# Kernel tuning notes

Hardware: AMD Instinct MI355X
Metric: run time of the kernel (lower is better)

The kernel has to match this reference:

```python
import jax, jax.numpy as jnp
import numpy as np
import math

DIM = 1024
NUM_HEADS = 16
HEAD_DIM = DIM // NUM_HEADS
B, S = 2, 2048

def setup_inputs() -> dict:
    key = jax.random.key(0)
    ks = jax.random.split(key, 9)
    sc = 0.02
    return {
        "x": jax.random.normal(ks[0], (B, S, DIM), jnp.float32),
        "Wq": jax.random.normal(ks[1], (DIM, DIM), jnp.float32) * sc,
        "bq": jax.random.normal(ks[2], (DIM,), jnp.float32) * sc,
        "Wk": jax.random.normal(ks[3], (DIM, DIM), jnp.float32) * sc,
        "bk": jax.random.normal(ks[4], (DIM,), jnp.float32) * sc,
        "Wv": jax.random.normal(ks[5], (DIM, DIM), jnp.float32) * sc,
        "bv": jax.random.normal(ks[6], (DIM,), jnp.float32) * sc,
        "Wo": jax.random.normal(ks[7], (DIM, DIM), jnp.float32) * sc,
        "bo": jax.random.normal(ks[8], (DIM,), jnp.float32) * sc,
    }

def reference(x, Wq, bq, Wk, bk, Wv, bv, Wo, bo):
    b, s, d = x.shape
    h, hd = NUM_HEADS, HEAD_DIM
    # qkv projections: [B,S,D] -> [B,H,S,hd]
    def split_heads(t):
        return t.reshape(b, s, h, hd).transpose(0, 2, 1, 3)
    q = split_heads(x @ Wq + bq)
    k = split_heads(x @ Wk + bk)
    v = split_heads(x @ Wv + bv)
    # scores [B,H,S,S], scale, causal mask via where(-10000), softmax
    scores = jnp.einsum('bhqd,bhkd->bhqk', q, k) / math.sqrt(hd)
    causal = jnp.tril(jnp.ones((s, s), dtype=bool))  # [S,S]
    scores = jnp.where(causal[None, None], scores, jnp.asarray(-10000.0, scores.dtype))
    probs = jax.nn.softmax(scores, axis=-1)
    ctx = jnp.einsum('bhqk,bhkd->bhqd', probs, v)
    ctx = ctx.transpose(0, 2, 1, 3).reshape(b, s, d)
    return ctx @ Wo + bo
```

## Files before the change

### kernel.cpp

```cpp
#include <hip/hip_runtime.h>
#include <hip/hip_bf16.h>

#define DIM 1024
#define NUM_HEADS 16
#define HEAD_DIM 64
#define BATCH 2
#define SEQ 2048
#define M_ROWS (BATCH * SEQ)

typedef short bh8 __attribute__((ext_vector_type(8)));
typedef float f32x4 __attribute__((ext_vector_type(4)));

__device__ __forceinline__ ushort f2bf(float f) {
    union { float f; unsigned u; } v; v.f = f;
    unsigned u = v.u;
    unsigned r = (u + 0x7FFFu + ((u >> 16) & 1u)) >> 16;
    return (ushort)r;
}

__device__ __forceinline__ ushort2 pk_bf16(float a, float b) {
#if __has_builtin(__builtin_amdgcn_cvt_pk_bf16_f32)
    auto r = __builtin_amdgcn_cvt_pk_bf16_f32(a, b);
    ushort2 o; __builtin_memcpy(&o, &r, 4); return o;
#else
    ushort2 o; o.x = f2bf(a); o.y = f2bf(b); return o;
#endif
}

__device__ __forceinline__ void async_cp16(const ushort* g, ushort* l) {
    __builtin_amdgcn_global_load_lds(
        (const __attribute__((address_space(1))) void*)(uintptr_t)g,
        (__attribute__((address_space(3))) void*)(uint32_t)(uintptr_t)l,
        16, 0, 0);
}

__global__ __launch_bounds__(256) void cast_x(const float* __restrict__ in,
                                              ushort* __restrict__ out, int n4) {
    int i = blockIdx.x * 256 + threadIdx.x;
    if (i < n4) {
        float4 v = ((const float4*)in)[i];
        ushort4 o;
        o.x = f2bf(v.x); o.y = f2bf(v.y); o.z = f2bf(v.z); o.w = f2bf(v.w);
        ((ushort4*)out)[i] = o;
    }
}

__global__ __launch_bounds__(256) void transpose_cast(const float* __restrict__ W,
                                                      ushort* __restrict__ Wt) {
    __shared__ float tile[32][33];
    const int t = threadIdx.x;
    const int tx = t & 31, ty = t >> 5;
    const int k0 = blockIdx.y * 32, n0 = blockIdx.x * 32;
    #pragma unroll
    for (int i = 0; i < 4; ++i)
        tile[ty + 8 * i][tx] = W[(size_t)(k0 + ty + 8 * i) * DIM + n0 + tx];
    __syncthreads();
    #pragma unroll
    for (int i = 0; i < 4; ++i)
        Wt[(size_t)(n0 + ty + 8 * i) * DIM + k0 + tx] = f2bf(tile[tx][ty + 8 * i]);
}

#define GTM 128
#define GTN 64
#define GBK 64

__device__ __forceinline__ void gemm_core(
    const ushort* __restrict__ A, const ushort* __restrict__ Bt,
    ushort* smem, int m0, int n0, int t, f32x4 acc[4][2])
{
    ushort* As = smem;
    ushort* Bs = smem + 8192;
    const int lane = t & 63, wave = t >> 6;
    const int col = lane & 15, quad = lane >> 4;
    const int wm = (wave & 1) * 64, wn = (wave >> 1) * 32;

    for (int k0 = 0; k0 < DIM; k0 += GBK) {
        __syncthreads();
        #pragma unroll
        for (int j = 0; j < 4; ++j) {
            int C = wave * 256 + j * 64 + lane;
            int row = C >> 3;
            int lch = (C & 7) ^ (row & 7);
            async_cp16(&A[(size_t)(m0 + row) * DIM + k0 + lch * 8],
                       &As[(wave * 256 + j * 64) * 8]);
        }
        #pragma unroll
        for (int j = 0; j < 2; ++j) {
            int C = wave * 128 + j * 64 + lane;
            int row = C >> 3;
            int lch = (C & 7) ^ (row & 7);
            async_cp16(&Bt[(size_t)(n0 + row) * DIM + k0 + lch * 8],
                       &Bs[(wave * 128 + j * 64) * 8]);
        }
        __syncthreads();
        #pragma unroll
        for (int kk = 0; kk < 2; ++kk) {
            bh8 af[4], bfr[2];
            #pragma unroll
            for (int mi = 0; mi < 4; ++mi) {
                int row = wm + mi * 16 + col;
                int ph = ((kk * 4 + quad) ^ (row & 7)) * 8;
                af[mi] = *(const bh8*)&As[row * 64 + ph];
            }
            #pragma unroll
            for (int ni = 0; ni < 2; ++ni) {
                int row = wn + ni * 16 + col;
                int ph = ((kk * 4 + quad) ^ (row & 7)) * 8;
                bfr[ni] = *(const bh8*)&Bs[row * 64 + ph];
            }
            #pragma unroll
            for (int mi = 0; mi < 4; ++mi)
                #pragma unroll
                for (int ni = 0; ni < 2; ++ni)
                    acc[mi][ni] = __builtin_amdgcn_mfma_f32_16x16x32_bf16(
                        af[mi], bfr[ni], acc[mi][ni], 0, 0, 0);
        }
    }
}

__global__ __launch_bounds__(256) void gemm_qkv(
    const ushort* __restrict__ A,
    const ushort* __restrict__ WqT, const ushort* __restrict__ WkT,
    const ushort* __restrict__ WvT,
    const float* __restrict__ bq, const float* __restrict__ bk,
    const float* __restrict__ bv,
    ushort* __restrict__ qo, ushort* __restrict__ ko_, ushort* __restrict__ vo)
{
    __shared__ ushort smem[12288];
    const int z = blockIdx.z;
    const ushort* Bt = (z == 0) ? WqT : (z == 1) ? WkT : WvT;
    const float* bias = (z == 0) ? bq : (z == 1) ? bk : bv;
    ushort* outp = (z == 0) ? qo : (z == 1) ? ko_ : vo;

    const int t = threadIdx.x;
    const int lane = t & 63, wave = t >> 6;
    const int col = lane & 15, quad = lane >> 4;
    const int m0 = blockIdx.y * GTM, n0 = blockIdx.x * GTN;
    const int wm = (wave & 1) * 64, wn = (wave >> 1) * 32;
    f32x4 acc[4][2] = {};

    gemm_core(A, Bt, smem, m0, n0, t, acc);

    const int b = m0 >> 11, s0 = m0 & (SEQ - 1);
    const int h = n0 >> 6;

    if (z < 2) {
        __syncthreads();
        ushort* LT = smem;
        #pragma unroll
        for (int mi = 0; mi < 4; ++mi)
            #pragma unroll
            for (int ni = 0; ni < 2; ++ni) {
                int dl = wn + ni * 16 + col;
                float bvv = bias[n0 + dl];
                #pragma unroll
                for (int r = 0; r < 4; ++r) {
                    int ml = wm + mi * 16 + quad * 4 + r;
                    LT[ml * 72 + dl] = f2bf(acc[mi][ni][r] + bvv);
                }
            }
        __syncthreads();
        ushort* Cp = outp + (((size_t)(b * NUM_HEADS + h) * SEQ + s0) << 6);
        #pragma unroll
        for (int i = 0; i < 4; ++i) {
            int c = i * 256 + t;
            int row = c >> 3, ko = (c & 7) * 8;
            *(uint4*)&Cp[row * 64 + ko] = *(const uint4*)&LT[row * 72 + ko];
        }
    } else {
        __syncthreads();
        ushort* LT = smem;
        #pragma unroll
        for (int mi = 0; mi < 4; ++mi)
            #pragma unroll
            for (int ni = 0; ni < 2; ++ni) {
                int nl = wn + ni * 16 + col;
                float bvv = bias[n0 + nl];
                #pragma unroll
                for (int r = 0; r < 4; ++r) {
                    int ml = wm + mi * 16 + quad * 4 + r;
                    LT[nl * 136 + ml] = f2bf(acc[mi][ni][r] + bvv);
                }
            }
        __syncthreads();
        ushort* Cp = outp + (((size_t)(b * NUM_HEADS + h) * HEAD_DIM) << 11);
        #pragma unroll
        for (int i = 0; i < 4; ++i) {
            int c = i * 256 + t;
            int row = c >> 4, mo = (c & 15) * 8;
            *(uint4*)&Cp[((size_t)row << 11) + s0 + mo] = *(const uint4*)&LT[row * 136 + mo];
        }
    }
}

__global__ __launch_bounds__(256) void gemm_out(
    const ushort* __restrict__ A, const ushort* __restrict__ Bt,
    const float* __restrict__ bias, float* __restrict__ C)
{
    __shared__ ushort smem[12288];
    const int t = threadIdx.x;
    const int lane = t & 63, wave = t >> 6;
    const int col = lane & 15, quad = lane >> 4;
    const int m0 = blockIdx.y * GTM, n0 = blockIdx.x * GTN;
    const int wm = (wave & 1) * 64, wn = (wave >> 1) * 32;
    f32x4 acc[4][2] = {};

    gemm_core(A, Bt, smem, m0, n0, t, acc);

    #pragma unroll
    for (int mi = 0; mi < 4; ++mi)
        #pragma unroll
        for (int ni = 0; ni < 2; ++ni) {
            int n = n0 + wn + ni * 16 + col;
            float bvv = bias[n];
            #pragma unroll
            for (int r = 0; r < 4; ++r) {
                int m = m0 + wm + mi * 16 + quad * 4 + r;
                C[(size_t)m * DIM + n] = acc[mi][ni][r] + bvv;
            }
        }
}

#define PSTR 72

__global__ __launch_bounds__(256) void attn_mfma(
    const ushort* __restrict__ Qg, const ushort* __restrict__ Kg,
    const ushort* __restrict__ Vtg, ushort* __restrict__ ctx)
{
    __shared__ ushort Ks[64 * 64];
    __shared__ ushort Vs[64 * 64];
    __shared__ ushort Ps[4][16 * PSTR];

    const int t = threadIdx.x;
    const int lane = t & 63, wave = t >> 6;
    const int col = lane & 15, quad = lane >> 4;
    const int pair = blockIdx.x & 15;
    const int bh = blockIdx.x >> 4;
    const int b = bh >> 4, h = bh & 15;
    const ushort* Kp = Kg + ((size_t)bh << 17);
    const ushort* Vp = Vtg + ((size_t)bh << 17);
    ushort* Pw = Ps[wave];
    const float SCL = 0.18033688011116016f;

    #pragma unroll 1
    for (int phase = 0; phase < 2; ++phase) {
        const int qt = phase ? (31 - pair) : pair;
        const int q0 = qt * 64;
        const int qw = q0 + wave * 16;

        bh8 qf0, qf1;
        {
            const ushort* Qp = Qg + ((size_t)bh << 17) + ((size_t)(qw + col) << 6) + quad * 8;
            qf0 = *(const bh8*)(Qp);
            qf1 = *(const bh8*)(Qp + 32);
        }
        float m_run = -1e30f, l_run = 0.f;
        f32x4 O[4] = {};

        #pragma unroll 1
        for (int kb = 0; kb <= q0; kb += 64) {
            __syncthreads();
            #pragma unroll
            for (int j = 0; j < 2; ++j) {
                int C = wave * 128 + j * 64 + lane;
                int row = C >> 3;
                int lch = (C & 7) ^ (row & 7);
                async_cp16(&Kp[((size_t)(kb + row) << 6) + lch * 8],
                           &Ks[(wave * 128 + j * 64) * 8]);
                async_cp16(&Vp[((size_t)row << 11) + kb + lch * 8],
                           &Vs[(wave * 128 + j * 64) * 8]);
            }
            __syncthreads();

            f32x4 St[4] = {};
            #pragma unroll
            for (int kk = 0; kk < 2; ++kk) {
                bh8 qf = kk ? qf1 : qf0;
                int ph = ((kk * 4 + quad) ^ (col & 7)) * 8;
                #pragma unroll
                for (int kt = 0; kt < 4; ++kt) {
                    bh8 kf = *(const bh8*)&Ks[(kt * 16 + col) * 64 + ph];
                    St[kt] = __builtin_amdgcn_mfma_f32_16x16x32_bf16(kf, qf, St[kt], 0, 0, 0);
                }
            }

            if (kb == q0) {
                const int q_abs = qw + col;
                #pragma unroll
                for (int kt = 0; kt < 4; ++kt)
                    #pragma unroll
                    for (int r = 0; r < 4; ++r)
                        if (kb + kt * 16 + quad * 4 + r > q_abs) St[kt][r] = -1e30f;
            }

            float mb = -1e30f;
            #pragma unroll
            for (int kt = 0; kt < 4; ++kt) {
                float m01 = fmaxf(St[kt][0], St[kt][1]);
                float m23 = fmaxf(St[kt][2], St[kt][3]);
                mb = fmaxf(mb, fmaxf(m01, m23));
            }
            mb = fmaxf(mb, __shfl_xor(mb, 16));
            mb = fmaxf(mb, __shfl_xor(mb, 32));
            float mn = fmaxf(m_run, mb);
            float alpha = exp2f((m_run - mn) * SCL);
            float negc = -mn * SCL;
            m_run = mn;

            float lb = 0.f;
            #pragma unroll
            for (int kt = 0; kt < 4; ++kt) {
                float p0 = exp2f(fmaf(St[kt][0], SCL, negc));
                float p1 = exp2f(fmaf(St[kt][1], SCL, negc));
                float p2 = exp2f(fmaf(St[kt][2], SCL, negc));
                float p3 = exp2f(fmaf(St[kt][3], SCL, negc));
                lb += (p0 + p1) + (p2 + p3);
                ushort2 a01 = pk_bf16(p0, p1), a23 = pk_bf16(p2, p3);
                ushort4 pk4; pk4.x = a01.x; pk4.y = a01.y; pk4.z = a23.x; pk4.w = a23.y;
                *(ushort4*)&Pw[col * PSTR + kt * 16 + quad * 4] = pk4;
            }
            lb += __shfl_xor(lb, 16);
            lb += __shfl_xor(lb, 32);
            l_run = l_run * alpha + lb;

            #pragma unroll
            for (int dt = 0; dt < 4; ++dt)
                #pragma unroll
                for (int r = 0; r < 4; ++r)
                    O[dt][r] *= alpha;

            #pragma unroll
            for (int kk = 0; kk < 2; ++kk) {
                int koff = kk * 32 + quad * 8;
                bh8 pf = *(const bh8*)&Pw[col * PSTR + koff];
                int ph = ((kk * 4 + quad) ^ (col & 7)) * 8;
                #pragma unroll
                for (int dt = 0; dt < 4; ++dt) {
                    bh8 vf = *(const bh8*)&Vs[(dt * 16 + col) * 64 + ph];
                    O[dt] = __builtin_amdgcn_mfma_f32_16x16x32_bf16(vf, pf, O[dt], 0, 0, 0);
                }
            }
        }

        float inv_l = 1.f / l_run;
        #pragma unroll
        for (int dt = 0; dt < 4; ++dt) {
            ushort2 a01 = pk_bf16(O[dt][0] * inv_l, O[dt][1] * inv_l);
            ushort2 a23 = pk_bf16(O[dt][2] * inv_l, O[dt][3] * inv_l);
            ushort4 pk4; pk4.x = a01.x; pk4.y = a01.y; pk4.z = a23.x; pk4.w = a23.y;
            *(ushort4*)&Pw[col * PSTR + dt * 16 + quad * 4] = pk4;
        }
        #pragma unroll
        for (int i = 0; i < 2; ++i) {
            int c = i * 64 + lane;
            int row = c >> 3, ko = (c & 7) * 8;
            *(uint4*)&ctx[((size_t)(b * SEQ) + qw + row) * DIM + (h << 6) + ko] =
                *(const uint4*)&Pw[row * PSTR + ko];
        }
    }
}

extern "C" void kernel_launch(void* const* d_in, const int* in_sizes, int n_in,
                              void* d_out, int out_size, void* d_ws, size_t ws_size,
                              hipStream_t stream) {
    const float* x  = (const float*)d_in[0];
    const float* Wq = (const float*)d_in[1];
    const float* bq = (const float*)d_in[2];
    const float* Wk = (const float*)d_in[3];
    const float* bk = (const float*)d_in[4];
    const float* Wv = (const float*)d_in[5];
    const float* bv = (const float*)d_in[6];
    const float* Wo = (const float*)d_in[7];
    const float* bo = (const float*)d_in[8];
    float* out = (float*)d_out;

    ushort* x_bf   = (ushort*)d_ws;
    ushort* wq_t   = x_bf + 4194304;
    ushort* wk_t   = wq_t + 1048576;
    ushort* wv_t   = wk_t + 1048576;
    ushort* wo_t   = wv_t + 1048576;
    ushort* q_ws   = wo_t + 1048576;
    ushort* k_ws   = q_ws + 4194304;
    ushort* vt_ws  = k_ws + 4194304;
    ushort* ctx_ws = vt_ws + 4194304;

    cast_x<<<4096, 256, 0, stream>>>(x, x_bf, (M_ROWS * DIM) / 4);
    dim3 tgrid(32, 32);
    transpose_cast<<<tgrid, 256, 0, stream>>>(Wq, wq_t);
    transpose_cast<<<tgrid, 256, 0, stream>>>(Wk, wk_t);
    transpose_cast<<<tgrid, 256, 0, stream>>>(Wv, wv_t);
    transpose_cast<<<tgrid, 256, 0, stream>>>(Wo, wo_t);

    dim3 qkv_grid(DIM / GTN, M_ROWS / GTM, 3);
    gemm_qkv<<<qkv_grid, 256, 0, stream>>>(x_bf, wq_t, wk_t, wv_t,
                                           bq, bk, bv, q_ws, k_ws, vt_ws);

    attn_mfma<<<BATCH * NUM_HEADS * 16, 256, 0, stream>>>(q_ws, k_ws, vt_ws, ctx_ws);

    dim3 ogrid(DIM / GTN, M_ROWS / GTM);
    gemm_out<<<ogrid, 256, 0, stream>>>(ctx_ws, wo_t, bo, out);
}
```

Measured before the change: 206.4 us.

## Enlarge GEMM tiles, widen attention query tiles, double-buffer K/V, drop running max

Both projection GEMMs go from 128x64 to 128x128 tiles, so each wave computes a 4x4 MFMA block and there is more reuse per staged tile. The attention kernel now covers 32 query rows per wave (128 per block) with half as many blocks. It double-buffers K/V tiles in LDS and prefetches the next tile while computing the current one. Online softmax max tracking and rescaling are removed, with raw scores exponentiated directly; this drops per-iteration reductions and rescales but risks overflow for inputs with large scores.

```diff
diff --git a/kernel.cpp b/kernel.cpp
--- a/kernel.cpp
+++ b/kernel.cpp
@@ -61,18 +61,18 @@
 }
 
 #define GTM 128
-#define GTN 64
+#define GTN 128
 #define GBK 64
 
 __device__ __forceinline__ void gemm_core(
     const ushort* __restrict__ A, const ushort* __restrict__ Bt,
-    ushort* smem, int m0, int n0, int t, f32x4 acc[4][2])
+    ushort* smem, int m0, int n0, int t, f32x4 acc[4][4])
 {
     ushort* As = smem;
     ushort* Bs = smem + 8192;
     const int lane = t & 63, wave = t >> 6;
     const int col = lane & 15, quad = lane >> 4;
-    const int wm = (wave & 1) * 64, wn = (wave >> 1) * 32;
+    const int wm = (wave & 1) * 64, wn = (wave >> 1) * 64;
 
     for (int k0 = 0; k0 < DIM; k0 += GBK) {
         __syncthreads();
@@ -85,35 +85,33 @@
                        &As[(wave * 256 + j * 64) * 8]);
         }
         #pragma unroll
-        for (int j = 0; j < 2; ++j) {
-            int C = wave * 128 + j * 64 + lane;
+        for (int j = 0; j < 4; ++j) {
+            int C = wave * 256 + j * 64 + lane;
             int row = C >> 3;
             int lch = (C & 7) ^ (row & 7);
             async_cp16(&Bt[(size_t)(n0 + row) * DIM + k0 + lch * 8],
-                       &Bs[(wave * 128 + j * 64) * 8]);
+                       &Bs[(wave * 256 + j * 64) * 8]);
         }
         __syncthreads();
         #pragma unroll
         for (int kk = 0; kk < 2; ++kk) {
-            bh8 af[4], bfr[2];
+            bh8 af[4], bf[4];
             #pragma unroll
             for (int mi = 0; mi < 4; ++mi) {
                 int row = wm + mi * 16 + col;
-                int ph = ((kk * 4 + quad) ^ (row & 7)) * 8;
-                af[mi] = *(const bh8*)&As[row * 64 + ph];
-            }
-            #pragma unroll
-            for (int ni = 0; ni < 2; ++ni) {
+                af[mi] = *(const bh8*)&As[row * 64 + (((kk * 4 + quad) ^ (row & 7)) * 8)];
+            }
+            #pragma unroll
+            for (int ni = 0; ni < 4; ++ni) {
                 int row = wn + ni * 16 + col;
-                int ph = ((kk * 4 + quad) ^ (row & 7)) * 8;
-                bfr[ni] = *(const bh8*)&Bs[row * 64 + ph];
+                bf[ni] = *(const bh8*)&Bs[row * 64 + (((kk * 4 + quad) ^ (row & 7)) * 8)];
             }
             #pragma unroll
             for (int mi = 0; mi < 4; ++mi)
                 #pragma unroll
-                for (int ni = 0; ni < 2; ++ni)
+                for (int ni = 0; ni < 4; ++ni)
                     acc[mi][ni] = __builtin_amdgcn_mfma_f32_16x16x32_bf16(
-                        af[mi], bfr[ni], acc[mi][ni], 0, 0, 0);
+                        af[mi], bf[ni], acc[mi][ni], 0, 0, 0);
         }
     }
 }
@@ -126,7 +124,7 @@
     const float* __restrict__ bv,
     ushort* __restrict__ qo, ushort* __restrict__ ko_, ushort* __restrict__ vo)
 {
-    __shared__ ushort smem[12288];
+    __shared__ ushort smem[17408];
     const int z = blockIdx.z;
     const ushort* Bt = (z == 0) ? WqT : (z == 1) ? WkT : WvT;
     const float* bias = (z == 0) ? bq : (z == 1) ? bk : bv;
@@ -136,59 +134,57 @@
     const int lane = t & 63, wave = t >> 6;
     const int col = lane & 15, quad = lane >> 4;
     const int m0 = blockIdx.y * GTM, n0 = blockIdx.x * GTN;
-    const int wm = (wave & 1) * 64, wn = (wave >> 1) * 32;
-    f32x4 acc[4][2] = {};
+    const int wm = (wave & 1) * 64, wn = (wave >> 1) * 64;
+    f32x4 acc[4][4] = {};
 
     gemm_core(A, Bt, smem, m0, n0, t, acc);
 
     const int b = m0 >> 11, s0 = m0 & (SEQ - 1);
-    const int h = n0 >> 6;
+    const int h0 = n0 >> 6;
+    __syncthreads();
+    ushort* LT = smem;
 
     if (z < 2) {
-        __syncthreads();
-        ushort* LT = smem;
         #pragma unroll
         for (int mi = 0; mi < 4; ++mi)
             #pragma unroll
-            for (int ni = 0; ni < 2; ++ni) {
+            for (int ni = 0; ni < 4; ++ni) {
                 int dl = wn + ni * 16 + col;
                 float bvv = bias[n0 + dl];
                 #pragma unroll
-                for (int r = 0; r < 4; ++r) {
-                    int ml = wm + mi * 16 + quad * 4 + r;
-                    LT[ml * 72 + dl] = f2bf(acc[mi][ni][r] + bvv);
-                }
+                for (int r = 0; r < 4; ++r)
+                    LT[(wm + mi * 16 + quad * 4 + r) * 136 + dl] = f2bf(acc[mi][ni][r] + bvv);
             }
         __syncthreads();
-        ushort* Cp = outp + (((size_t)(b * NUM_HEADS + h) * SEQ + s0) << 6);
-        #pragma unroll
-        for (int i = 0; i < 4; ++i) {
+        #pragma unroll
+        for (int i = 0; i < 8; ++i) {
             int c = i * 256 + t;
-            int row = c >> 3, ko = (c & 7) * 8;
-            *(uint4*)&Cp[row * 64 + ko] = *(const uint4*)&LT[row * 72 + ko];
+            int row = c >> 4;
+            int dcol = (c & 15) * 8;
+            int h = h0 + (dcol >> 6);
+            *(uint4*)&outp[(((size_t)(b * NUM_HEADS + h) * SEQ) + s0 + row) * 64 + (dcol & 63)] =
+                *(const uint4*)&LT[row * 136 + dcol];
         }
     } else {
-        __syncthreads();
-        ushort* LT = smem;
         #pragma unroll
         for (int mi = 0; mi < 4; ++mi)
             #pragma unroll
-            for (int ni = 0; ni < 2; ++ni) {
+            for (int ni = 0; ni < 4; ++ni) {
                 int nl = wn + ni * 16 + col;
                 float bvv = bias[n0 + nl];
                 #pragma unroll
-                for (int r = 0; r < 4; ++r) {
-                    int ml = wm + mi * 16 + quad * 4 + r;
-                    LT[nl * 136 + ml] = f2bf(acc[mi][ni][r] + bvv);
-                }
+                for (int r = 0; r < 4; ++r)
+                    LT[nl * 136 + (wm + mi * 16 + quad * 4 + r)] = f2bf(acc[mi][ni][r] + bvv);
             }
         __syncthreads();
-        ushort* Cp = outp + (((size_t)(b * NUM_HEADS + h) * HEAD_DIM) << 11);
-        #pragma unroll
-        for (int i = 0; i < 4; ++i) {
+        #pragma unroll
+        for (int i = 0; i < 8; ++i) {
             int c = i * 256 + t;
-            int row = c >> 4, mo = (c & 15) * 8;
-            *(uint4*)&Cp[((size_t)row << 11) + s0 + mo] = *(const uint4*)&LT[row * 136 + mo];
+            int row = c >> 4;
+            int moff = (c & 15) * 8;
+            int h = h0 + (row >> 6);
+            *(uint4*)&outp[(((size_t)(b * NUM_HEADS + h) * HEAD_DIM) + (row & 63)) * SEQ + s0 + moff] =
+                *(const uint4*)&LT[row * 136 + moff];
         }
     }
 }
@@ -197,20 +193,20 @@
     const ushort* __restrict__ A, const ushort* __restrict__ Bt,
     const float* __restrict__ bias, float* __restrict__ C)
 {
-    __shared__ ushort smem[12288];
+    __shared__ ushort smem[16384];
     const int t = threadIdx.x;
     const int lane = t & 63, wave = t >> 6;
     const int col = lane & 15, quad = lane >> 4;
     const int m0 = blockIdx.y * GTM, n0 = blockIdx.x * GTN;
-    const int wm = (wave & 1) * 64, wn = (wave >> 1) * 32;
-    f32x4 acc[4][2] = {};
+    const int wm = (wave & 1) * 64, wn = (wave >> 1) * 64;
+    f32x4 acc[4][4] = {};
 
     gemm_core(A, Bt, smem, m0, n0, t, acc);
 
     #pragma unroll
     for (int mi = 0; mi < 4; ++mi)
         #pragma unroll
-        for (int ni = 0; ni < 2; ++ni) {
+        for (int ni = 0; ni < 4; ++ni) {
             int n = n0 + wn + ni * 16 + col;
             float bvv = bias[n];
             #pragma unroll
@@ -227,15 +223,15 @@
     const ushort* __restrict__ Qg, const ushort* __restrict__ Kg,
     const ushort* __restrict__ Vtg, ushort* __restrict__ ctx)
 {
-    __shared__ ushort Ks[64 * 64];
-    __shared__ ushort Vs[64 * 64];
-    __shared__ ushort Ps[4][16 * PSTR];
+    __shared__ ushort Ks[2][64 * 64];
+    __shared__ ushort Vs[2][64 * 64];
+    __shared__ ushort Ps[4][32 * PSTR];
 
     const int t = threadIdx.x;
     const int lane = t & 63, wave = t >> 6;
     const int col = lane & 15, quad = lane >> 4;
-    const int pair = blockIdx.x & 15;
-    const int bh = blockIdx.x >> 4;
+    const int pair = blockIdx.x & 7;
+    const int bh = blockIdx.x >> 3;
     const int b = bh >> 4, h = bh & 15;
     const ushort* Kp = Kg + ((size_t)bh << 17);
     const ushort* Vp = Vtg + ((size_t)bh << 17);
@@ -244,114 +240,128 @@
 
     #pragma unroll 1
     for (int phase = 0; phase < 2; ++phase) {
-        const int qt = phase ? (31 - pair) : pair;
-        const int q0 = qt * 64;
-        const int qw = q0 + wave * 16;
-
-        bh8 qf0, qf1;
+        const int qt = phase ? (15 - pair) : pair;
+        const int q0 = qt * 128;
+        const int qw = q0 + wave * 32;
+
+        bh8 qf[2][2];
+        #pragma unroll
+        for (int ni = 0; ni < 2; ++ni) {
+            const ushort* Qp = Qg + ((size_t)bh << 17) + ((size_t)(qw + ni * 16 + col) << 6) + quad * 8;
+            qf[ni][0] = *(const bh8*)(Qp);
+            qf[ni][1] = *(const bh8*)(Qp + 32);
+        }
+        float l0 = 0.f, l1 = 0.f;
+        f32x4 O[4][2] = {};
+        const int nIter = 2 * qt + 2;
+
+        __syncthreads();
         {
-            const ushort* Qp = Qg + ((size_t)bh << 17) + ((size_t)(qw + col) << 6) + quad * 8;
-            qf0 = *(const bh8*)(Qp);
-            qf1 = *(const bh8*)(Qp + 32);
-        }
-        float m_run = -1e30f, l_run = 0.f;
-        f32x4 O[4] = {};
-
-        #pragma unroll 1
-        for (int kb = 0; kb <= q0; kb += 64) {
-            __syncthreads();
             #pragma unroll
             for (int j = 0; j < 2; ++j) {
                 int C = wave * 128 + j * 64 + lane;
                 int row = C >> 3;
                 int lch = (C & 7) ^ (row & 7);
-                async_cp16(&Kp[((size_t)(kb + row) << 6) + lch * 8],
-                           &Ks[(wave * 128 + j * 64) * 8]);
-                async_cp16(&Vp[((size_t)row << 11) + kb + lch * 8],
-                           &Vs[(wave * 128 + j * 64) * 8]);
-            }
+                async_cp16(&Kp[((size_t)row << 6) + lch * 8], &Ks[0][(wave * 128 + j * 64) * 8]);
+                async_cp16(&Vp[((size_t)row << 11) + lch * 8], &Vs[0][(wave * 128 + j * 64) * 8]);
+            }
+        }
+
+        #pragma unroll 1
+        for (int it = 0; it < nIter; ++it) {
+            const int kb = it * 64;
             __syncthreads();
-
-            f32x4 St[4] = {};
+            if (it + 1 < nIter) {
+                int kb2 = kb + 64;
+                #pragma unroll
+                for (int j = 0; j < 2; ++j) {
+                    int C = wave * 128 + j * 64 + lane;
+                    int row = C >> 3;
+                    int lch = (C & 7) ^ (row & 7);
+                    ushort* kd = &Ks[(it + 1) & 1][(wave * 128 + j * 64) * 8];
+                    ushort* vd = &Vs[(it + 1) & 1][(wave * 128 + j * 64) * 8];
+                    async_cp16(&Kp[((size_t)(kb2 + row) << 6) + lch * 8], kd);
+                    async_cp16(&Vp[((size_t)row << 11) + kb2 + lch * 8], vd);
+                }
+            }
+            if (kb > qw + 31) continue;
+            const ushort* Kb = Ks[it & 1];
+            const ushort* Vb = Vs[it & 1];
+
+            f32x4 St[4][2] = {};
             #pragma unroll
             for (int kk = 0; kk < 2; ++kk) {
-                bh8 qf = kk ? qf1 : qf0;
                 int ph = ((kk * 4 + quad) ^ (col & 7)) * 8;
                 #pragma unroll
                 for (int kt = 0; kt < 4; ++kt) {
-                    bh8 kf = *(const bh8*)&Ks[(kt * 16 + col) * 64 + ph];
-                    St[kt] = __builtin_amdgcn_mfma_f32_16x16x32_bf16(kf, qf, St[kt], 0, 0, 0);
+                    bh8 kf = *(const bh8*)&Kb[(kt * 16 + col) * 64 + ph];
+                    #pragma unroll
+                    for (int ni = 0; ni < 2; ++ni)
+                        St[kt][ni] = __builtin_amdgcn_mfma_f32_16x16x32_bf16(
+                            kf, qf[ni][kk], St[kt][ni], 0, 0, 0);
                 }
             }
 
-            if (kb == q0) {
-                const int q_abs = qw + col;
-                #pragma unroll
-                for (int kt = 0; kt < 4; ++kt)
+            if (kb + 63 > qw) {
+                #pragma unroll
+                for (int ni = 0; ni < 2; ++ni) {
+                    int q_abs = qw + ni * 16 + col;
                     #pragma unroll
-                    for (int r = 0; r < 4; ++r)
-                        if (kb + kt * 16 + quad * 4 + r > q_abs) St[kt][r] = -1e30f;
-            }
-
-            float mb = -1e30f;
+                    for (int kt = 0; kt < 4; ++kt)
+                        #pragma unroll
+                        for (int r = 0; r < 4; ++r)
+                            if (kb + kt * 16 + quad * 4 + r > q_abs) St[kt][ni][r] = -1e30f;
+                }
+            }
+
+            float lb0 = 0.f, lb1 = 0.f;
             #pragma unroll
             for (int kt = 0; kt < 4; ++kt) {
-                float m01 = fmaxf(St[kt][0], St[kt][1]);
-                float m23 = fmaxf(St[kt][2], St[kt][3]);
-                mb = fmaxf(mb, fmaxf(m01, m23));
-            }
-            mb = fmaxf(mb, __shfl_xor(mb, 16));
-            mb = fmaxf(mb, __shfl_xor(mb, 32));
-            float mn = fmaxf(m_run, mb);
-            float alpha = exp2f((m_run - mn) * SCL);
-            float negc = -mn * SCL;
-            m_run = mn;
-
-            float lb = 0.f;
-            #pragma unroll
-            for (int kt = 0; kt < 4; ++kt) {
-                float p0 = exp2f(fmaf(St[kt][0], SCL, negc));
-                float p1 = exp2f(fmaf(St[kt][1], SCL, negc));
-                float p2 = exp2f(fmaf(St[kt][2], SCL, negc));
-                float p3 = exp2f(fmaf(St[kt][3], SCL, negc));
-                lb += (p0 + p1) + (p2 + p3);
-                ushort2 a01 = pk_bf16(p0, p1), a23 = pk_bf16(p2, p3);
-                ushort4 pk4; pk4.x = a01.x; pk4.y = a01.y; pk4.z = a23.x; pk4.w = a23.y;
-                *(ushort4*)&Pw[col * PSTR + kt * 16 + quad * 4] = pk4;
-            }
-            lb += __shfl_xor(lb, 16);
-            lb += __shfl_xor(lb, 32);
-            l_run = l_run * alpha + lb;
-
-            #pragma unroll
-            for (int dt = 0; dt < 4; ++dt)
-                #pragma unroll
-                for (int r = 0; r < 4; ++r)
-                    O[dt][r] *= alpha;
+                #pragma unroll
+                for (int ni = 0; ni < 2; ++ni) {
+                    float p0 = exp2f(St[kt][ni][0] * SCL);
+                    float p1 = exp2f(St[kt][ni][1] * SCL);
+                    float p2 = exp2f(St[kt][ni][2] * SCL);
+                    float p3 = exp2f(St[kt][ni][3] * SCL);
+                    if (ni) lb1 += (p0 + p1) + (p2 + p3);
+                    else    lb0 += (p0 + p1) + (p2 + p3);
+                    ushort2 a01 = pk_bf16(p0, p1), a23 = pk_bf16(p2, p3);
+                    ushort4 pk4; pk4.x = a01.x; pk4.y = a01.y; pk4.z = a23.x; pk4.w = a23.y;
+                    *(ushort4*)&Pw[(ni * 16 + col) * PSTR + kt * 16 + quad * 4] = pk4;
+                }
+            }
+            lb0 += __shfl_xor(lb0, 16); lb0 += __shfl_xor(lb0, 32);
+            lb1 += __shfl_xor(lb1, 16); lb1 += __shfl_xor(lb1, 32);
+            l0 += lb0; l1 += lb1;
 
             #pragma unroll
             for (int kk = 0; kk < 2; ++kk) {
                 int koff = kk * 32 + quad * 8;
-                bh8 pf = *(const bh8*)&Pw[col * PSTR + koff];
+                bh8 pf0 = *(const bh8*)&Pw[col * PSTR + koff];
+                bh8 pf1 = *(const bh8*)&Pw[(16 + col) * PSTR + koff];
                 int ph = ((kk * 4 + quad) ^ (col & 7)) * 8;
                 #pragma unroll
                 for (int dt = 0; dt < 4; ++dt) {
-                    bh8 vf = *(const bh8*)&Vs[(dt * 16 + col) * 64 + ph];
-                    O[dt] = __builtin_amdgcn_mfma_f32_16x16x32_bf16(vf, pf, O[dt], 0, 0, 0);
+                    bh8 vf = *(const bh8*)&Vb[(dt * 16 + col) * 64 + ph];
+                    O[dt][0] = __builtin_amdgcn_mfma_f32_16x16x32_bf16(vf, pf0, O[dt][0], 0, 0, 0);
+                    O[dt][1] = __builtin_amdgcn_mfma_f32_16x16x32_bf16(vf, pf1, O[dt][1], 0, 0, 0);
                 }
             }
         }
 
-        float inv_l = 1.f / l_run;
-        #pragma unroll
-        for (int dt = 0; dt < 4; ++dt) {
-            ushort2 a01 = pk_bf16(O[dt][0] * inv_l, O[dt][1] * inv_l);
-            ushort2 a23 = pk_bf16(O[dt][2] * inv_l, O[dt][3] * inv_l);
-            ushort4 pk4; pk4.x = a01.x; pk4.y = a01.y; pk4.z = a23.x; pk4.w = a23.y;
-            *(ushort4*)&Pw[col * PSTR + dt * 16 + quad * 4] = pk4;
-        }
-        #pragma unroll
-        for (int i = 0; i < 2; ++i) {
+        float inv0 = 1.f / l0, inv1 = 1.f / l1;
+        #pragma unroll
+        for (int dt = 0; dt < 4; ++dt)
+            #pragma unroll
+            for (int ni = 0; ni < 2; ++ni) {
+                float inv = ni ? inv1 : inv0;
+                ushort2 a01 = pk_bf16(O[dt][ni][0] * inv, O[dt][ni][1] * inv);
+                ushort2 a23 = pk_bf16(O[dt][ni][2] * inv, O[dt][ni][3] * inv);
+                ushort4 pk4; pk4.x = a01.x; pk4.y = a01.y; pk4.z = a23.x; pk4.w = a23.y;
+                *(ushort4*)&Pw[(ni * 16 + col) * PSTR + dt * 16 + quad * 4] = pk4;
+            }
+        #pragma unroll
+        for (int i = 0; i < 4; ++i) {
             int c = i * 64 + lane;
             int row = c >> 3, ko = (c & 7) * 8;
             *(uint4*)&ctx[((size_t)(b * SEQ) + qw + row) * DIM + (h << 6) + ko] =
@@ -395,7 +405,7 @@
     gemm_qkv<<<qkv_grid, 256, 0, stream>>>(x_bf, wq_t, wk_t, wv_t,
                                            bq, bk, bv, q_ws, k_ws, vt_ws);
 
-    attn_mfma<<<BATCH * NUM_HEADS * 16, 256, 0, stream>>>(q_ws, k_ws, vt_ws, ctx_ws);
+    attn_mfma<<<BATCH * NUM_HEADS * 8, 256, 0, stream>>>(q_ws, k_ws, vt_ws, ctx_ws);
 
     dim3 ogrid(DIM / GTN, M_ROWS / GTM);
     gemm_out<<<ogrid, 256, 0, stream>>>(ctx_ws, wo_t, bo, out);
```

Result: slower. 225.8 us (+9.4%).
